# Performance work log

Measured on AMD Instinct MI355X. Metric: run time of the kernel, lower is better.

## Reference

```python
import jax, jax.numpy as jnp
import numpy as np

N = 3072          # num nodes
E = 49152         # num edges (avg degree 16)
D = 256           # hidden_dim
O = 512           # output_dim
H = 8             # num_heads
DH = D // H       # head_dim = 32
NET = 5           # num_edge_types
NC = 8            # num_communities
L_LOC = 2         # num_local_layers
L_GLB = 2         # num_global_layers


def _layernorm(x, g, b, eps=1e-5):
    m = jnp.mean(x, axis=-1, keepdims=True)
    v = jnp.mean((x - m) ** 2, axis=-1, keepdims=True)
    return (x - m) * jax.lax.rsqrt(v + eps) * g + b


def setup_inputs() -> dict:
    key = jax.random.key(0)
    ks = jax.random.split(key, 40)
    s = 0.02
    inp = {
        "x": jax.random.normal(ks[0], (N, 1), jnp.float32),
        "edge_index": jax.random.randint(ks[1], (2, E), 0, N),
        "edge_types": jax.random.randint(ks[2], (E,), 0, NET),
        "pos_encoding": jax.random.normal(ks[3], (N, D), jnp.float32),
        "community_ids": jax.random.randint(ks[4], (N,), 0, NC),
        "adj_matrix": jnp.zeros((N, N), jnp.float32),
        # node embedding Linear(1, D)
        "emb_w": jax.random.normal(ks[5], (1, D)) * s,
        "emb_b": jnp.zeros((D,)),
        # local (Graphormer) layers, stacked over L_LOC
        "loc_qw": jax.random.normal(ks[6], (L_LOC, D, D)) * s,
        "loc_qb": jnp.zeros((L_LOC, D)),
        "loc_kw": jax.random.normal(ks[7], (L_LOC, D, D)) * s,
        "loc_kb": jnp.zeros((L_LOC, D)),
        "loc_vw": jax.random.normal(ks[8], (L_LOC, D, D)) * s,
        "loc_vb": jnp.zeros((L_LOC, D)),
        "loc_ow": jax.random.normal(ks[9], (L_LOC, D, D)) * s,
        "loc_ob": jnp.zeros((L_LOC, D)),
        "loc_eb": jax.random.normal(ks[10], (L_LOC, NET, H)) * s,  # edge-type attn bias per head
        "loc_ln_g": jnp.ones((L_LOC, D)),
        "loc_ln_b": jnp.zeros((L_LOC, D)),
        # global interaction layers, stacked over L_GLB
        "glob_qw": jax.random.normal(ks[11], (L_GLB, D, D)) * s,
        "glob_qb": jnp.zeros((L_GLB, D)),
        "glob_kw": jax.random.normal(ks[12], (L_GLB, D, D)) * s,
        "glob_kb": jnp.zeros((L_GLB, D)),
        "glob_vw": jax.random.normal(ks[13], (L_GLB, D, D)) * s,
        "glob_vb": jnp.zeros((L_GLB, D)),
        "glob_ow": jax.random.normal(ks[14], (L_GLB, D, D)) * s,
        "glob_ob": jnp.zeros((L_GLB, D)),
        "glob_ln_g": jnp.ones((L_GLB, D)),
        "glob_ln_b": jnp.zeros((L_GLB, D)),
        # output projection
        "out_w": jax.random.normal(ks[15], (D, O)) * s,
        "out_b": jnp.zeros((O,)),
    }
    return inp


def reference(x, edge_index, edge_types, pos_encoding, community_ids, adj_matrix,
              emb_w, emb_b,
              loc_qw, loc_qb, loc_kw, loc_kb, loc_vw, loc_vb, loc_ow, loc_ob,
              loc_eb, loc_ln_g, loc_ln_b,
              glob_qw, glob_qb, glob_kw, glob_kb, glob_vw, glob_vb,
              glob_ow, glob_ob, glob_ln_g, glob_ln_b,
              out_w, out_b):
    n = x.shape[0]
    h = x @ emb_w + emb_b                                  # [N, D]
    same = community_ids[:, None] == community_ids[None, :]  # [N, N] same-community mask
    src, dst = edge_index[0], edge_index[1]

    # Local layers: the original per-community subgraph loop (with full attention
    # inside each community) is mathematically a single masked full attention
    # restricted to same-community pairs, with edge-type bias at graph edges.
    for l in range(loc_qw.shape[0]):
        hp = h + pos_encoding
        q = (hp @ loc_qw[l] + loc_qb[l]).reshape(n, H, DH)
        k = (hp @ loc_kw[l] + loc_kb[l]).reshape(n, H, DH)
        v = (hp @ loc_vw[l] + loc_vb[l]).reshape(n, H, DH)
        # edge-type attention bias, scattered at edges  -> [H, N, N]
        bias = jnp.zeros((H, n, n), dtype=h.dtype).at[:, src, dst].add(loc_eb[l][edge_types].T)
        scores = jnp.einsum('nhd,mhd->hnm', q, k) / np.sqrt(DH) + bias
        scores = jnp.where(same[None, :, :], scores, -jnp.inf)  # attend within community only
        attn = jax.nn.softmax(scores, axis=-1)
        o = jnp.einsum('hnm,mhd->nhd', attn, v).reshape(n, D)
        h = _layernorm(h + o @ loc_ow[l] + loc_ob[l], loc_ln_g[l], loc_ln_b[l])

    # Global interaction: attend only to nodes in *different* communities
    for g in range(glob_qw.shape[0]):
        Q = h @ glob_qw[g] + glob_qb[g]
        K = h @ glob_kw[g] + glob_kb[g]
        V = h @ glob_vw[g] + glob_vb[g]
        scores = (Q @ K.T) / np.sqrt(DH)                   # scaled by head_dim as in source
        scores = jnp.where(~same, scores, -jnp.inf)        # mask same-community (incl. self)
        attn = jax.nn.softmax(scores, axis=-1)
        o = (attn @ V) @ glob_ow[g] + glob_ob[g]
        h = _layernorm(o + h, glob_ln_g[g], glob_ln_b[g])

    return h @ out_w + out_b                               # [N, O]
```

## Files before the change

### kernel.cpp

```cpp
#include <hip/hip_runtime.h>
#include <hip/hip_bf16.h>
#include <stdint.h>

#define NN 3072
#define EE 49152
#define DD 256
#define OO 512
#define HH 8
#define DHH 32
#define NETT 5
#define NC 8
#define NCMAX 512
#define SCP 516
#define KS 16
#define NW 17

typedef __attribute__((ext_vector_type(8))) short short8;
typedef __attribute__((ext_vector_type(4))) float f32x4;

__device__ __forceinline__ short f2bf_s(float f){
    __hip_bfloat16 h = __float2bfloat16(f);
    return *reinterpret_cast<short*>(&h);
}
__device__ __forceinline__ float bf2f_s(short v){
    __hip_bfloat16 h;
    *reinterpret_cast<short*>(&h) = v;
    return __bfloat162float(h);
}

__global__ void k_embed(const float* __restrict__ x, const float* __restrict__ w,
                        const float* __restrict__ b, const float* __restrict__ pos,
                        float* __restrict__ h, short* __restrict__ hbf, short* __restrict__ hpbf){
    int i = blockIdx.x * 256 + threadIdx.x;
    int n = i >> 8, d = i & 255;
    float v = x[n] * w[d] + b[d];
    h[i] = v;
    hbf[i] = f2bf_s(v);
    hpbf[i] = f2bf_s(v + pos[i]);
}

__global__ __launch_bounds__(256) void k_vtrans(const float* __restrict__ v, short* __restrict__ vt){
    __shared__ float t[32][33];
    int bx = blockIdx.x;
    int by = blockIdx.y;
    int lx = threadIdx.x & 31, ly = threadIdx.x >> 5;
    for (int i = ly; i < 32; i += 8)
        t[i][lx] = v[(size_t)(bx * 32 + i) * DD + by * 32 + lx];
    __syncthreads();
    for (int r = ly; r < 32; r += 8)
        vt[(size_t)(by * 32 + r) * NN + bx * 32 + lx] = f2bf_s(t[lx][r]);
}

__global__ __launch_bounds__(256) void k_vtrans_sorted(const float* __restrict__ v,
                                                       const int* __restrict__ perm,
                                                       short* __restrict__ vt){
    __shared__ float t[32][33];
    int bx = blockIdx.x;
    int by = blockIdx.y;
    int lx = threadIdx.x & 31, ly = threadIdx.x >> 5;
    for (int i = ly; i < 32; i += 8)
        t[i][lx] = v[(size_t)perm[bx * 32 + i] * DD + by * 32 + lx];
    __syncthreads();
    for (int r = ly; r < 32; r += 8)
        vt[(size_t)(by * 32 + r) * NN + bx * 32 + lx] = f2bf_s(t[lx][r]);
}

struct WT {
    const float* src[NW];
    short*       dst[NW];
    int          M[NW];
};
__global__ __launch_bounds__(256) void k_wtrans(WT wt){
    int id = blockIdx.z;
    int M = wt.M[id];
    int bx = blockIdx.x;
    if (bx * 32 >= M) return;
    int by = blockIdx.y;
    __shared__ float t[32][33];
    int lx = threadIdx.x & 31, ly = threadIdx.x >> 5;
    const float* w = wt.src[id];
    for (int i = ly; i < 32; i += 8)
        t[i][lx] = w[(size_t)(by * 32 + i) * M + bx * 32 + lx];
    __syncthreads();
    short* d = wt.dst[id];
    for (int r = ly; r < 32; r += 8)
        d[(size_t)(bx * 32 + r) * DD + by * 32 + lx] = f2bf_s(t[lx][r]);
}

__global__ void k_count(const int* __restrict__ ei, int* __restrict__ cnt){
    int e = blockIdx.x * 256 + threadIdx.x;
    if (e < EE) atomicAdd(&cnt[ei[e]], 1);
}

__global__ void k_scan(const int* __restrict__ cnt, int* __restrict__ rp){
    __shared__ int part[256];
    int tid = threadIdx.x;
    int base = tid * 12;
    int loc[12]; int s = 0;
    for (int i = 0; i < 12; i++){ loc[i] = s; s += cnt[base + i]; }
    part[tid] = s; __syncthreads();
    if (tid == 0){ int a = 0; for (int i = 0; i < 256; i++){ int t = part[i]; part[i] = a; a += t; } }
    __syncthreads();
    int b = part[tid];
    for (int i = 0; i < 12; i++) rp[base + i] = b + loc[i];
    if (tid == 255) rp[NN] = b + s;
}

__global__ void k_fill(const int* __restrict__ ei, const int* __restrict__ et,
                       const int* __restrict__ rp, int* __restrict__ cur,
                       int* __restrict__ e_dst, int* __restrict__ e_typ){
    int e = blockIdx.x * 256 + threadIdx.x;
    if (e < EE){
        int s = ei[e], d = ei[EE + e];
        int p = atomicAdd(&cur[s], 1);
        int idx = rp[s] + p;
        e_dst[idx] = d; e_typ[idx] = et[e];
    }
}

__global__ void k_ccount(const int* __restrict__ comm, int* __restrict__ ccnt){
    int n = blockIdx.x * 256 + threadIdx.x;
    if (n < NN) atomicAdd(&ccnt[comm[n]], 1);
}

__global__ void k_cscan(const int* __restrict__ ccnt, int* __restrict__ cstart){
    cstart[0] = 0;
    for (int c = 0; c < NC; c++) cstart[c + 1] = cstart[c] + ccnt[c];
}

__global__ void k_cfill(const int* __restrict__ comm, const int* __restrict__ cstart,
                        int* __restrict__ ccur, int* __restrict__ perm, int* __restrict__ inv){
    int n = blockIdx.x * 256 + threadIdx.x;
    if (n < NN){
        int c = comm[n];
        int p = cstart[c] + atomicAdd(&ccur[c], 1);
        perm[p] = n; inv[n] = p;
    }
}

template<int M>
__global__ __launch_bounds__(256) void k_gemm_mfma(
        const short* __restrict__ A, const short* __restrict__ Wt,
        const float* __restrict__ bias, float* __restrict__ C){
    int tid = threadIdx.x;
    int w = tid >> 6, lane = tid & 63, quad = lane >> 4, col = lane & 15;
    int m0 = blockIdx.x * 64 + w * 16;
    int n0 = blockIdx.y * 64;

    const short* arow = A + (size_t)(m0 + col) * DD;

    f32x4 acc[4];
    #pragma unroll
    for (int su = 0; su < 4; su++) acc[su] = (f32x4){0.f, 0.f, 0.f, 0.f};

    #pragma unroll
    for (int f = 0; f < 8; f++){
        int k0 = f * 32 + quad * 8;
        short8 af = *(const short8*)(arow + k0);
        #pragma unroll
        for (int su = 0; su < 4; su++){
            short8 bf = *(const short8*)(Wt + (size_t)(n0 + su * 16 + col) * DD + k0);
            acc[su] = __builtin_amdgcn_mfma_f32_16x16x32_bf16(af, bf, acc[su], 0, 0, 0);
        }
    }

    #pragma unroll
    for (int su = 0; su < 4; su++){
        int n = n0 + su * 16 + col;
        float bz = bias[n];
        #pragma unroll
        for (int r = 0; r < 4; r++)
            C[(size_t)(m0 + quad * 4 + r) * M + n] = acc[su][r] + bz;
    }
}

struct QKV {
    const short* Wt[3];
    const float* bias[3];
    float*       Cf[3];
    short*       Cb[3];
};
__global__ __launch_bounds__(256) void k_gemm_qkv(
        const short* __restrict__ A, QKV q, const int* __restrict__ inv){
    int z = blockIdx.z;
    const short* Wt = q.Wt[z];
    const float* bias = q.bias[z];
    float* Cf = q.Cf[z];
    short* Cb = q.Cb[z];

    int tid = threadIdx.x;
    int w = tid >> 6, lane = tid & 63, quad = lane >> 4, col = lane & 15;
    int m0 = blockIdx.x * 64 + w * 16;
    int n0 = blockIdx.y * 64;

    const short* arow = A + (size_t)(m0 + col) * DD;

    f32x4 acc[4];
    #pragma unroll
    for (int su = 0; su < 4; su++) acc[su] = (f32x4){0.f, 0.f, 0.f, 0.f};

    #pragma unroll
    for (int f = 0; f < 8; f++){
        int k0 = f * 32 + quad * 8;
        short8 af = *(const short8*)(arow + k0);
        #pragma unroll
        for (int su = 0; su < 4; su++){
            short8 bf = *(const short8*)(Wt + (size_t)(n0 + su * 16 + col) * DD + k0);
            acc[su] = __builtin_amdgcn_mfma_f32_16x16x32_bf16(af, bf, acc[su], 0, 0, 0);
        }
    }

    #pragma unroll
    for (int su = 0; su < 4; su++){
        int n = n0 + su * 16 + col;
        float bz = bias[n];
        #pragma unroll
        for (int r = 0; r < 4; r++){
            float val = acc[su][r] + bz;
            int m = m0 + quad * 4 + r;
            if (Cf) Cf[(size_t)m * DD + n] = val;
            if (Cb){
                int ms = inv ? inv[m] : m;
                Cb[(size_t)ms * DD + n] = f2bf_s(val);
            }
        }
    }
}

__global__ __launch_bounds__(256) void k_gemm_o_ln(
        const short* __restrict__ A, const short* __restrict__ Wt,
        const float* __restrict__ bias,
        const float* __restrict__ g, const float* __restrict__ b,
        const float* __restrict__ pos,
        float* __restrict__ h, short* __restrict__ hbf, short* __restrict__ hpbf){
    __shared__ float t[16][258];
    int tid = threadIdx.x;
    int w = tid >> 6, lane = tid & 63, quad = lane >> 4, col = lane & 15;
    int m0 = blockIdx.x * 16;
    int n0 = w * 64;

    const short* arow = A + (size_t)(m0 + col) * DD;

    f32x4 acc[4];
    #pragma unroll
    for (int su = 0; su < 4; su++) acc[su] = (f32x4){0.f, 0.f, 0.f, 0.f};

    #pragma unroll
    for (int f = 0; f < 8; f++){
        int k0 = f * 32 + quad * 8;
        short8 af = *(const short8*)(arow + k0);
        #pragma unroll
        for (int su = 0; su < 4; su++){
            short8 bf = *(const short8*)(Wt + (size_t)(n0 + su * 16 + col) * DD + k0);
            acc[su] = __builtin_amdgcn_mfma_f32_16x16x32_bf16(af, bf, acc[su], 0, 0, 0);
        }
    }

    #pragma unroll
    for (int su = 0; su < 4; su++){
        int n = n0 + su * 16 + col;
        float bz = bias[n];
        #pragma unroll
        for (int r = 0; r < 4; r++)
            t[quad * 4 + r][n] = acc[su][r] + bz;
    }
    __syncthreads();

    int row = tid >> 4, l16 = tid & 15;
    int m = m0 + row;
    float v[16];
    float s = 0.f;
    #pragma unroll
    for (int j = 0; j < 16; j++){
        int d = l16 + j * 16;
        float vv = t[row][d] + h[(size_t)m * DD + d];
        v[j] = vv; s += vv;
    }
    #pragma unroll
    for (int off = 1; off < 16; off <<= 1) s += __shfl_xor(s, off);
    float mean = s * (1.0f / 256.0f);
    float s2 = 0.f;
    #pragma unroll
    for (int j = 0; j < 16; j++){ float c = v[j] - mean; s2 += c * c; }
    #pragma unroll
    for (int off = 1; off < 16; off <<= 1) s2 += __shfl_xor(s2, off);
    float rstd = rsqrtf(s2 * (1.0f / 256.0f) + 1e-5f);
    #pragma unroll
    for (int j = 0; j < 16; j++){
        int d = l16 + j * 16;
        float out = (v[j] - mean) * rstd * g[d] + b[d];
        size_t idx = (size_t)m * DD + d;
        h[idx] = out;
        hbf[idx] = f2bf_s(out);
        if (pos) hpbf[idx] = f2bf_s(out + pos[idx]);
    }
}

__global__ __launch_bounds__(256) void k_local_attn6(
        const short* __restrict__ Qs, const short* __restrict__ Ks, const short* __restrict__ Vts,
        const int* __restrict__ cstart, const int* __restrict__ perm, const int* __restrict__ inv,
        const int* __restrict__ rp, const int* __restrict__ e_dst, const int* __restrict__ e_typ,
        const float* __restrict__ eb, short* __restrict__ obbf){
    int c  = blockIdx.y;
    int hh = blockIdx.z;
    int cs0 = cstart[c], cs1 = cstart[c + 1];
    int Nc = cs1 - cs0;
    int p0 = blockIdx.x * 16;
    if (p0 >= Nc) return;
    int tid = threadIdx.x;
    int w = tid >> 6, lane = tid & 63, quad = lane >> 4, col = lane & 15;
    int nt  = (Nc + 15) >> 4;
    int nt2 = (Nc + 31) >> 5;

    __shared__ float sc[16][SCP];
    __shared__ float linv[16];
    __shared__ int qnode[16];

    if (tid < 16) qnode[tid] = (p0 + tid < Nc) ? perm[cs0 + p0 + tid] : -1;

    int qrow = cs0 + min(p0 + col, Nc - 1);
    short8 qf = *(const short8*)(Qs + (size_t)qrow * DD + hh * DHH + quad * 8);

    const float scale = 0.17677669529663687f;

    for (int t = w; t < nt; t += 4){
        int kt = t * 16;
        int krow = cs0 + min(kt + col, Nc - 1);
        short8 kf = *(const short8*)(Ks + (size_t)krow * DD + hh * DHH + quad * 8);
        f32x4 s = __builtin_amdgcn_mfma_f32_16x16x32_bf16(qf, kf, (f32x4){0.f,0.f,0.f,0.f}, 0, 0, 0);
        #pragma unroll
        for (int r = 0; r < 4; r++)
            sc[quad * 4 + r][kt + col] = s[r] * scale;
    }
    __syncthreads();

    int qi = tid >> 4, l16 = tid & 15;
    {
        int n = qnode[qi];
        if (n >= 0){
            int re = rp[n + 1];
            for (int e2 = rp[n] + l16; e2 < re; e2 += 16){
                int dpos = inv[e_dst[e2]];
                if (dpos >= cs0 && dpos < cs1)
                    atomicAdd(&sc[qi][dpos - cs0], eb[e_typ[e2] * HH + hh]);
            }
        }
    }
    __syncthreads();

    {
        float lm = -1e30f;
        for (int m = l16; m < Nc; m += 16) lm = fmaxf(lm, sc[qi][m]);
        #pragma unroll
        for (int off = 1; off < 16; off <<= 1) lm = fmaxf(lm, __shfl_xor(lm, off));
        float ls = 0.f;
        for (int m = l16; m < Nc; m += 16){
            float e_ = __expf(sc[qi][m] - lm);
            sc[qi][m] = e_;
            ls += e_;
        }
        for (int m = (Nc & ~15) + l16; m < nt2 * 32; m += 16)
            if (m >= Nc) sc[qi][m] = 0.f;
        #pragma unroll
        for (int off = 1; off < 16; off <<= 1) ls += __shfl_xor(ls, off);
        if (l16 == 0) linv[qi] = 1.f / ls;
    }
    __syncthreads();

    f32x4 acc0 = (f32x4){0.f,0.f,0.f,0.f}, acc1 = (f32x4){0.f,0.f,0.f,0.f};
    for (int t2 = w; t2 < nt2; t2 += 4){
        int kt = t2 * 32;
        float4 pa = *(const float4*)&sc[col][kt + quad * 8];
        float4 pb = *(const float4*)&sc[col][kt + quad * 8 + 4];
        short8 pf;
        pf[0] = f2bf_s(pa.x); pf[1] = f2bf_s(pa.y); pf[2] = f2bf_s(pa.z); pf[3] = f2bf_s(pa.w);
        pf[4] = f2bf_s(pb.x); pf[5] = f2bf_s(pb.y); pf[6] = f2bf_s(pb.z); pf[7] = f2bf_s(pb.w);
        const short* vb0 = Vts + (size_t)(hh * DHH + col) * NN + cs0 + kt + quad * 8;
        short8 vf0 = *(const short8*)(vb0);
        short8 vf1 = *(const short8*)(vb0 + (size_t)16 * NN);
        acc0 = __builtin_amdgcn_mfma_f32_16x16x32_bf16(pf, vf0, acc0, 0, 0, 0);
        acc1 = __builtin_amdgcn_mfma_f32_16x16x32_bf16(pf, vf1, acc1, 0, 0, 0);
    }
    __syncthreads();
    {
        float (*pv)[16][33] = reinterpret_cast<float (*)[16][33]>(&sc[0][0]);
        #pragma unroll
        for (int r = 0; r < 4; r++){
            pv[w][quad * 4 + r][col]      = acc0[r];
            pv[w][quad * 4 + r][col + 16] = acc1[r];
        }
        __syncthreads();

        int q = tid >> 4, d0 = tid & 15;
        int n = qnode[q];
        #pragma unroll
        for (int half = 0; half < 2; half++){
            int dd = d0 + half * 16;
            float sum = pv[0][q][dd] + pv[1][q][dd] + pv[2][q][dd] + pv[3][q][dd];
            if (n >= 0) obbf[(size_t)n * DD + hh * DHH + dd] = f2bf_s(sum * linv[q]);
        }
    }
}

__global__ __launch_bounds__(256) void k_glob_mfma9(
        const short* __restrict__ Qb, const short* __restrict__ Kb,
        const short* __restrict__ Vt, const int* __restrict__ comm,
        short* __restrict__ Opart, float* __restrict__ lpart){
    int tid = threadIdx.x;
    int w = tid >> 6, lane = tid & 63, quad = lane >> 4, col = lane & 15;
    int qt = blockIdx.x * 64 + w * 16;
    int split = blockIdx.y;
    int ks0 = split * (NN / KS);

    __shared__ __align__(16) short Kl[32][264];
    __shared__ __align__(16) short Vl[256][40];
    __shared__ __align__(16) short Pl[4][16][40];

    short8 qf[8];
    #pragma unroll
    for (int f = 0; f < 8; f++)
        qf[f] = *(const short8*)(Qb + (size_t)(qt + col) * DD + f * 32 + quad * 8);

    int qc[4];
    #pragma unroll
    for (int r = 0; r < 4; r++) qc[r] = comm[qt + quad * 4 + r];

    f32x4 accO[16];
    #pragma unroll
    for (int dt = 0; dt < 16; dt++) accO[dt] = (f32x4){0.f, 0.f, 0.f, 0.f};
    float l_[4] = {0.f, 0.f, 0.f, 0.f};

    const float scale = 0.17677669529663687f;

    for (int t = 0; t < NN / KS / 32; t++){
        int kt = ks0 + t * 32;
        __syncthreads();
        #pragma unroll
        for (int i = 0; i < 4; i++){
            int idx = tid + i * 256;
            int row = idx >> 5, seg = idx & 31;
            *(short8*)&Kl[row][seg * 8] = *(const short8*)(Kb + (size_t)(kt + row) * DD + seg * 8);
        }
        #pragma unroll
        for (int i = 0; i < 4; i++){
            int idx = tid + i * 256;
            int d = idx >> 2, seg = idx & 3;
            *(short8*)&Vl[d][seg * 8] = *(const short8*)(Vt + (size_t)d * NN + kt + seg * 8);
        }
        __syncthreads();

        f32x4 s0 = (f32x4){0.f,0.f,0.f,0.f}, s1 = (f32x4){0.f,0.f,0.f,0.f};
        #pragma unroll
        for (int f = 0; f < 8; f++){
            short8 kf0 = *(const short8*)&Kl[col][f * 32 + quad * 8];
            short8 kf1 = *(const short8*)&Kl[16 + col][f * 32 + quad * 8];
            s0 = __builtin_amdgcn_mfma_f32_16x16x32_bf16(qf[f], kf0, s0, 0, 0, 0);
            s1 = __builtin_amdgcn_mfma_f32_16x16x32_bf16(qf[f], kf1, s1, 0, 0, 0);
        }

        int cm0 = comm[kt + col], cm1 = comm[kt + 16 + col];
        #pragma unroll
        for (int r = 0; r < 4; r++){
            float p0 = (cm0 != qc[r]) ? __expf(s0[r] * scale) : 0.f;
            float p1 = (cm1 != qc[r]) ? __expf(s1[r] * scale) : 0.f;
            l_[r] += p0 + p1;
            int row = quad * 4 + r;
            Pl[w][row][col]      = f2bf_s(p0);
            Pl[w][row][col + 16] = f2bf_s(p1);
        }
        short8 pf = *(const short8*)(&Pl[w][col][quad * 8]);
        #pragma unroll
        for (int dt = 0; dt < 16; dt++){
            short8 vf = *(const short8*)&Vl[dt * 16 + col][quad * 8];
            accO[dt] = __builtin_amdgcn_mfma_f32_16x16x32_bf16(pf, vf, accO[dt], 0, 0, 0);
        }
    }

    #pragma unroll
    for (int r = 0; r < 4; r++){
        float vv = l_[r];
        #pragma unroll
        for (int off = 1; off < 16; off <<= 1) vv += __shfl_xor(vv, off);
        l_[r] = vv;
    }

    #pragma unroll
    for (int r = 0; r < 4; r++){
        int row = qt + quad * 4 + r;
        if (col == 0) lpart[split * NN + row] = l_[r];
        #pragma unroll
        for (int dt = 0; dt < 16; dt++)
            Opart[((size_t)split * NN + row) * DD + dt * 16 + col] = f2bf_s(accO[dt][r]);
    }
}

__global__ __launch_bounds__(256) void k_gmerge(
        const short* __restrict__ Opart, const float* __restrict__ lpart,
        short* __restrict__ obbf){
    int qn = blockIdx.x, d = threadIdx.x;
    float l = 0.f, val = 0.f;
    #pragma unroll
    for (int s = 0; s < KS; s++){
        l += lpart[s * NN + qn];
        val += bf2f_s(Opart[((size_t)s * NN + qn) * DD + d]);
    }
    obbf[(size_t)qn * DD + d] = f2bf_s(val / l);
}

extern "C" void kernel_launch(void* const* d_in, const int* in_sizes, int n_in,
                              void* d_out, int out_size, void* d_ws, size_t ws_size,
                              hipStream_t stream){
    const float* x        = (const float*)d_in[0];
    const int*   ei       = (const int*)  d_in[1];
    const int*   et       = (const int*)  d_in[2];
    const float* pos      = (const float*)d_in[3];
    const int*   comm     = (const int*)  d_in[4];
    const float* emb_w    = (const float*)d_in[6];
    const float* emb_b    = (const float*)d_in[7];
    const float* loc_qw   = (const float*)d_in[8];
    const float* loc_qb   = (const float*)d_in[9];
    const float* loc_kw   = (const float*)d_in[10];
    const float* loc_kb   = (const float*)d_in[11];
    const float* loc_vw   = (const float*)d_in[12];
    const float* loc_vb   = (const float*)d_in[13];
    const float* loc_ow   = (const float*)d_in[14];
    const float* loc_ob   = (const float*)d_in[15];
    const float* loc_eb   = (const float*)d_in[16];
    const float* loc_ln_g = (const float*)d_in[17];
    const float* loc_ln_b = (const float*)d_in[18];
    const float* glob_qw  = (const float*)d_in[19];
    const float* glob_qb  = (const float*)d_in[20];
    const float* glob_kw  = (const float*)d_in[21];
    const float* glob_kb  = (const float*)d_in[22];
    const float* glob_vw  = (const float*)d_in[23];
    const float* glob_vb  = (const float*)d_in[24];
    const float* glob_ow  = (const float*)d_in[25];
    const float* glob_ob  = (const float*)d_in[26];
    const float* glob_ln_g= (const float*)d_in[27];
    const float* glob_ln_b= (const float*)d_in[28];
    const float* out_w    = (const float*)d_in[29];
    const float* out_b    = (const float*)d_in[30];

    float* h    = (float*)d_ws;
    float* vb_  = h    + NN * DD;
    float* lpart= vb_  + NN * DD;
    int* cnt    = (int*)(lpart + KS * NN);
    int* cur    = cnt + NN;
    int* ccnt   = cur + NN;
    int* ccur   = ccnt + NC;
    int* cstart = ccur + NC;
    int* rp     = cstart + NC + 1;
    int* perm   = rp + NN + 1;
    int* inv    = perm + NN;
    int* e_dst  = inv + NN;
    int* e_typ  = e_dst + EE;
    short* Qbf  = (short*)(((uintptr_t)(e_typ + EE) + 15) & ~(uintptr_t)15);
    short* Kbf  = Qbf + NN * DD;
    short* Vt   = Kbf + NN * DD;
    short* WtAll= Vt + (size_t)DD * NN;
    short* Qs   = WtAll + 16 * DD * DD + DD * OO;
    short* Ks2  = Qs + (size_t)NN * DD;
    short* Vts  = Ks2 + (size_t)NN * DD;
    short* Opart= Vts + (size_t)DD * NN;
    short* hbf  = Opart + (size_t)KS * NN * DD;
    short* hpbf = hbf + (size_t)NN * DD;
    short* obbf = hpbf + (size_t)NN * DD;

    WT wt;
    const float* wsrc[NW] = {
        loc_qw, loc_kw, loc_vw, loc_ow,
        loc_qw + DD * DD, loc_kw + DD * DD, loc_vw + DD * DD, loc_ow + DD * DD,
        glob_qw, glob_kw, glob_vw, glob_ow,
        glob_qw + DD * DD, glob_kw + DD * DD, glob_vw + DD * DD, glob_ow + DD * DD,
        out_w };
    for (int i = 0; i < NW; i++){
        wt.src[i] = wsrc[i];
        wt.dst[i] = WtAll + (size_t)i * DD * DD;
        wt.M[i]   = (i == 16) ? OO : DD;
    }
    short* WtLQ[2] = { WtAll + 0 * DD * DD, WtAll + 4 * DD * DD };
    short* WtLK[2] = { WtAll + 1 * DD * DD, WtAll + 5 * DD * DD };
    short* WtLV[2] = { WtAll + 2 * DD * DD, WtAll + 6 * DD * DD };
    short* WtLO[2] = { WtAll + 3 * DD * DD, WtAll + 7 * DD * DD };
    short* WtGQ[2] = { WtAll + 8 * DD * DD, WtAll + 12 * DD * DD };
    short* WtGK[2] = { WtAll + 9 * DD * DD, WtAll + 13 * DD * DD };
    short* WtGV[2] = { WtAll + 10 * DD * DD, WtAll + 14 * DD * DD };
    short* WtGO[2] = { WtAll + 11 * DD * DD, WtAll + 15 * DD * DD };
    short* WtOut   = WtAll + 16 * DD * DD;

    (void)hipMemsetAsync(cnt, 0, sizeof(int) * (2 * NN + 2 * NC), stream);

    k_embed<<<NN * DD / 256, 256, 0, stream>>>(x, emb_w, emb_b, pos, h, hbf, hpbf);
    k_wtrans<<<dim3(16, 8, NW), 256, 0, stream>>>(wt);
    k_count<<<EE / 256, 256, 0, stream>>>(ei, cnt);
    k_scan<<<1, 256, 0, stream>>>(cnt, rp);
    k_fill<<<EE / 256, 256, 0, stream>>>(ei, et, rp, cur, e_dst, e_typ);
    k_ccount<<<NN / 256, 256, 0, stream>>>(comm, ccnt);
    k_cscan<<<1, 1, 0, stream>>>(ccnt, cstart);
    k_cfill<<<NN / 256, 256, 0, stream>>>(comm, cstart, ccur, perm, inv);

    for (int l = 0; l < 2; l++){
        QKV q;
        q.Wt[0] = WtLQ[l]; q.Wt[1] = WtLK[l]; q.Wt[2] = WtLV[l];
        q.bias[0] = loc_qb + l * DD; q.bias[1] = loc_kb + l * DD; q.bias[2] = loc_vb + l * DD;
        q.Cf[0] = nullptr; q.Cf[1] = nullptr; q.Cf[2] = vb_;
        q.Cb[0] = Qs; q.Cb[1] = Ks2; q.Cb[2] = nullptr;
        k_gemm_qkv<<<dim3(NN / 64, DD / 64, 3), 256, 0, stream>>>(hpbf, q, inv);
        k_vtrans_sorted<<<dim3(NN / 32, DD / 32), 256, 0, stream>>>(vb_, perm, Vts);
        k_local_attn6<<<dim3(NCMAX / 16, NC, HH), 256, 0, stream>>>(
            Qs, Ks2, Vts, cstart, perm, inv, rp, e_dst, e_typ,
            loc_eb + l * NETT * HH, obbf);
        k_gemm_o_ln<<<NN / 16, 256, 0, stream>>>(
            obbf, WtLO[l], loc_ob + l * DD, loc_ln_g + l * DD, loc_ln_b + l * DD,
            (l == 0) ? pos : nullptr, h, hbf, hpbf);
    }

    for (int g = 0; g < 2; g++){
        QKV q;
        q.Wt[0] = WtGQ[g]; q.Wt[1] = WtGK[g]; q.Wt[2] = WtGV[g];
        q.bias[0] = glob_qb + g * DD; q.bias[1] = glob_kb + g * DD; q.bias[2] = glob_vb + g * DD;
        q.Cf[0] = nullptr; q.Cf[1] = nullptr; q.Cf[2] = vb_;
        q.Cb[0] = Qbf; q.Cb[1] = Kbf; q.Cb[2] = nullptr;
        k_gemm_qkv<<<dim3(NN / 64, DD / 64, 3), 256, 0, stream>>>(hbf, q, nullptr);
        k_vtrans<<<dim3(NN / 32, DD / 32), 256, 0, stream>>>(vb_, Vt);
        k_glob_mfma9<<<dim3(NN / 64, KS), 256, 0, stream>>>(Qbf, Kbf, Vt, comm, Opart, lpart);
        k_gmerge<<<NN, 256, 0, stream>>>(Opart, lpart, obbf);
        k_gemm_o_ln<<<NN / 16, 256, 0, stream>>>(
            obbf, WtGO[g], glob_ob + g * DD, glob_ln_g + g * DD, glob_ln_b + g * DD,
            nullptr, h, hbf, nullptr);
    }

    k_gemm_mfma<OO><<<dim3(NN / 64, OO / 64), 256, 0, stream>>>(hbf, WtOut, out_b, (float*)d_out);
}
```

Measured before the change: 503.7 us.

## Prefetch next K/V tile into registers and XOR-swizzle K shared layout

The global attention kernel now loads the next K and V tiles into registers while the current tile is being computed, which overlaps global memory latency with MFMA work. The K tile in shared memory drops its padding and uses an XOR swizzle on the column offset to avoid bank conflicts. Register pressure rises from the eight extra short8 prefetch buffers, which could reduce occupancy.

```diff
diff --git a/kernel.cpp b/kernel.cpp
--- a/kernel.cpp
+++ b/kernel.cpp
@@ -402,7 +402,7 @@
     }
 }
 
-__global__ __launch_bounds__(256) void k_glob_mfma9(
+__global__ __launch_bounds__(256) void k_glob_mfma10(
         const short* __restrict__ Qb, const short* __restrict__ Kb,
         const short* __restrict__ Vt, const int* __restrict__ comm,
         short* __restrict__ Opart, float* __restrict__ lpart){
@@ -411,8 +411,9 @@
     int qt = blockIdx.x * 64 + w * 16;
     int split = blockIdx.y;
     int ks0 = split * (NN / KS);
-
-    __shared__ __align__(16) short Kl[32][264];
+    const int NT = NN / KS / 32;
+
+    __shared__ __align__(16) short Kl[32 * 256];
     __shared__ __align__(16) short Vl[256][40];
     __shared__ __align__(16) short Pl[4][16][40];
 
@@ -432,28 +433,44 @@
 
     const float scale = 0.17677669529663687f;
 
-    for (int t = 0; t < NN / KS / 32; t++){
+    int ksg = tid & 31;
+    int kr0 = tid >> 5;
+    int ksw = (kr0 & 7) << 3;
+    int vsg = tid & 3;
+    int vd0 = tid >> 2;
+
+    short8 kpre[4], vpre[4];
+    #pragma unroll
+    for (int i = 0; i < 4; i++){
+        kpre[i] = *(const short8*)(Kb + (size_t)(ks0 + kr0 + 8 * i) * DD + ksg * 8);
+        vpre[i] = *(const short8*)(Vt + (size_t)(vd0 + 64 * i) * NN + ks0 + vsg * 8);
+    }
+
+    for (int t = 0; t < NT; t++){
         int kt = ks0 + t * 32;
         __syncthreads();
         #pragma unroll
         for (int i = 0; i < 4; i++){
-            int idx = tid + i * 256;
-            int row = idx >> 5, seg = idx & 31;
-            *(short8*)&Kl[row][seg * 8] = *(const short8*)(Kb + (size_t)(kt + row) * DD + seg * 8);
-        }
-        #pragma unroll
-        for (int i = 0; i < 4; i++){
-            int idx = tid + i * 256;
-            int d = idx >> 2, seg = idx & 3;
-            *(short8*)&Vl[d][seg * 8] = *(const short8*)(Vt + (size_t)d * NN + kt + seg * 8);
+            *(short8*)&Kl[(kr0 + 8 * i) * 256 + ((ksg * 8) ^ ksw)] = kpre[i];
+            *(short8*)&Vl[vd0 + 64 * i][vsg * 8] = vpre[i];
         }
         __syncthreads();
+        if (t + 1 < NT){
+            int kn = kt + 32;
+            #pragma unroll
+            for (int i = 0; i < 4; i++){
+                kpre[i] = *(const short8*)(Kb + (size_t)(kn + kr0 + 8 * i) * DD + ksg * 8);
+                vpre[i] = *(const short8*)(Vt + (size_t)(vd0 + 64 * i) * NN + kn + vsg * 8);
+            }
+        }
 
         f32x4 s0 = (f32x4){0.f,0.f,0.f,0.f}, s1 = (f32x4){0.f,0.f,0.f,0.f};
+        int csw = (col & 7) << 3;
         #pragma unroll
         for (int f = 0; f < 8; f++){
-            short8 kf0 = *(const short8*)&Kl[col][f * 32 + quad * 8];
-            short8 kf1 = *(const short8*)&Kl[16 + col][f * 32 + quad * 8];
+            int cs = (f * 32 + quad * 8) ^ csw;
+            short8 kf0 = *(const short8*)&Kl[col * 256 + cs];
+            short8 kf1 = *(const short8*)&Kl[(16 + col) * 256 + cs];
             s0 = __builtin_amdgcn_mfma_f32_16x16x32_bf16(qf[f], kf0, s0, 0, 0, 0);
             s1 = __builtin_amdgcn_mfma_f32_16x16x32_bf16(qf[f], kf1, s1, 0, 0, 0);
         }
@@ -623,7 +640,7 @@
         q.Cb[0] = Qbf; q.Cb[1] = Kbf; q.Cb[2] = nullptr;
         k_gemm_qkv<<<dim3(NN / 64, DD / 64, 3), 256, 0, stream>>>(hbf, q, nullptr);
         k_vtrans<<<dim3(NN / 32, DD / 32), 256, 0, stream>>>(vb_, Vt);
-        k_glob_mfma9<<<dim3(NN / 64, KS), 256, 0, stream>>>(Qbf, Kbf, Vt, comm, Opart, lpart);
+        k_glob_mfma10<<<dim3(NN / 64, KS), 256, 0, stream>>>(Qbf, Kbf, Vt, comm, Opart, lpart);
         k_gmerge<<<NN, 256, 0, stream>>>(Opart, lpart, obbf);
         k_gemm_o_ln<<<NN / 16, 256, 0, stream>>>(
             obbf, WtGO[g], glob_ob + g * DD, glob_ln_g + g * DD, glob_ln_b + g * DD,
```

Result: no change. 499.1 us (-0.9%).
